# Kernel optimization log

Hardware: AMD Instinct MI355X
Metric: run time of the kernel (lower is better)

## Reference

```python
import jax, jax.numpy as jnp
import numpy as np

B, T, S, E = 32, 32, 8, 512
H, D, FF, NL = 8, 64, 2048, 4
AEMB, NACT = 64, 18
L = T * S            # qlen = 256
MEM = 256
KLEN = L + MEM       # 512


def _ln(x, g, b, eps=1e-5):
    m = jnp.mean(x, -1, keepdims=True)
    v = jnp.mean(jnp.square(x - m), -1, keepdims=True)
    return (x - m) * jax.lax.rsqrt(v + eps) * g + b


def _rel_shift(bd):
    # bd: [qlen, klen, B, H] -- TransformerXL rel-shift trick
    q, k, b, h = bd.shape
    bd = jnp.pad(bd, ((0, 0), (1, 0), (0, 0), (0, 0)))
    return bd.reshape(k + 1, q, b, h)[1:].reshape(q, k, b, h)


def setup_inputs() -> dict:
    key = jax.random.key(0)
    ks = jax.random.split(key, 20)
    s = 0.02  # weight init scale
    x = jax.random.normal(ks[0], (B, T, S, E), jnp.float32)
    action = jax.random.randint(ks[1], (B, T), 0, NACT, dtype=jnp.int32)
    i = jnp.arange(L)[:, None]
    j = jnp.arange(KLEN)[None, :]
    attn_mask = j > (i + MEM)                      # True = masked (causal w/ memory)
    positions = jnp.arange(KLEN - 1, -1, -1, dtype=jnp.int32)  # TXL descending positions
    mems = jax.random.normal(ks[2], (NL, MEM, B, E), jnp.float32) * 0.1
    return {
        'x': x, 'action': action, 'attn_mask': attn_mask, 'positions': positions,
        'mems': mems,
        'act_emb': jax.random.normal(ks[3], (NACT, AEMB), jnp.float32) * s,
        'stem_w1': jax.random.normal(ks[4], (E + AEMB, E), jnp.float32) * s,
        'stem_ln1_g': jnp.ones((E,), jnp.float32), 'stem_ln1_b': jnp.zeros((E,), jnp.float32),
        'stem_w2': jax.random.normal(ks[5], (E, E), jnp.float32) * s,
        'stem_ln2_g': jnp.ones((E,), jnp.float32), 'stem_ln2_b': jnp.zeros((E,), jnp.float32),
        'lnf_g': jnp.ones((E,), jnp.float32), 'lnf_b': jnp.zeros((E,), jnp.float32),
        'u_bias': jax.random.normal(ks[6], (H, D), jnp.float32) * s,
        'v_bias': jax.random.normal(ks[7], (H, D), jnp.float32) * s,
        'Wqkv': jax.random.normal(ks[8], (NL, E, 3 * H * D), jnp.float32) * s,
        'Wr': jax.random.normal(ks[9], (NL, E, H * D), jnp.float32) * s,
        'Wo': jax.random.normal(ks[10], (NL, H * D, E), jnp.float32) * s,
        'ln1_g': jnp.ones((NL, E), jnp.float32), 'ln1_b': jnp.zeros((NL, E), jnp.float32),
        'W1': jax.random.normal(ks[11], (NL, E, FF), jnp.float32) * s,
        'b1': jnp.zeros((NL, FF), jnp.float32),
        'W2': jax.random.normal(ks[12], (NL, FF, E), jnp.float32) * s,
        'b2': jnp.zeros((NL, E), jnp.float32),
        'ln2_g': jnp.ones((NL, E), jnp.float32), 'ln2_b': jnp.zeros((NL, E), jnp.float32),
    }


def reference(x, action, attn_mask, positions, mems, act_emb,
              stem_w1, stem_ln1_g, stem_ln1_b, stem_w2, stem_ln2_g, stem_ln2_b,
              lnf_g, lnf_b, u_bias, v_bias, Wqkv, Wr, Wo,
              ln1_g, ln1_b, W1, b1, W2, b2, ln2_g, ln2_b):
    Bv, Tv, Sv, Ev = x.shape
    Hh, Dd = u_bias.shape
    qlen = Tv * Sv
    # --- stem (StateMixer, concat type) ---
    xs = x.reshape(Bv, qlen, Ev).transpose(1, 0, 2)                # [L,B,E] time-major
    a = act_emb[action]                                            # [B,T,AEMB]
    a = jnp.repeat(a, Sv, axis=1).transpose(1, 0, 2)               # [L,B,AEMB]
    h = jnp.concatenate([xs, a], -1) @ stem_w1
    h = jax.nn.relu(_ln(h, stem_ln1_g, stem_ln1_b))
    h = _ln(h @ stem_w2, stem_ln2_g, stem_ln2_b)
    feats = _ln(h, lnf_g, lnf_b, eps=1e-6)
    # --- sinusoidal positional encoding of relative positions ---
    pf = positions.astype(jnp.float32)
    inv = 1.0 / (10000.0 ** (jnp.arange(0, Ev, 2, dtype=jnp.float32) / Ev))
    ang = pf[:, None] * inv[None, :]
    pos_emb = jnp.concatenate([jnp.sin(ang), jnp.cos(ang)], -1)    # [KLEN,E]
    scale = 1.0 / np.sqrt(Dd)
    out = feats
    for l in range(Wqkv.shape[0]):
        cat = jnp.concatenate([mems[l], out], 0)                   # [klen,B,E]
        klen = cat.shape[0]
        q, k, v = jnp.split(cat @ Wqkv[l], 3, -1)
        q = q[-qlen:].reshape(qlen, Bv, Hh, Dd)
        k = k.reshape(klen, Bv, Hh, Dd)
        v = v.reshape(klen, Bv, Hh, Dd)
        r = (pos_emb @ Wr[l]).reshape(klen, Hh, Dd)
        AC = jnp.einsum('ibhd,jbhd->ijbh', q + u_bias, k)
        BD = _rel_shift(jnp.einsum('ibhd,jhd->ijbh', q + v_bias, r))
        score = (AC + BD) * scale
        score = jnp.where(attn_mask[:, :, None, None], jnp.float32(-1e30), score)
        attn = jax.nn.softmax(score, axis=1)
        ao = jnp.einsum('ijbh,jbhd->ibhd', attn, v).reshape(qlen, Bv, Hh * Dd) @ Wo[l]
        h1 = _ln(out + ao, ln1_g[l], ln1_b[l])
        ff = jax.nn.relu(h1 @ W1[l] + b1[l]) @ W2[l] + b2[l]
        out = _ln(h1 + ff, ln2_g[l], ln2_b[l])
    return out.transpose(1, 0, 2).reshape(Bv, Tv, Sv, Ev)
```

## Files before the change

### kernel.cpp

```cpp
#include <hip/hip_runtime.h>


typedef __attribute__((ext_vector_type(8))) short bf8_t;
typedef __attribute__((ext_vector_type(4))) float f4_t;
typedef __attribute__((ext_vector_type(16))) float fx16;

__device__ __forceinline__ ushort f2bf(float f) {
    uint u = __float_as_uint(f);
    u += 0x7FFFu + ((u >> 16) & 1u);
    return (ushort)(u >> 16);
}
__device__ __forceinline__ float b2f(ushort h) {
    return __uint_as_float(((uint)h) << 16);
}
__device__ __forceinline__ void gload16(const void* g, void* l) {
    __builtin_amdgcn_global_load_lds((const __attribute__((address_space(1))) void*)g,
                                     (__attribute__((address_space(3))) void*)l, 16, 0, 0);
}
__device__ __forceinline__ void xcd_tiles(int& mt, int& nt) {
    const int gx = gridDim.x;
    const int flat = (int)blockIdx.y * gx + (int)blockIdx.x;
    const int q = (gx * gridDim.y) >> 3;
    const int swz = (flat & 7) * q + (flat >> 3);
    nt = swz % gx;
    mt = swz / gx;
}

__device__ __forceinline__ void mma32_step(const ushort* __restrict__ As,
                                           const ushort* __restrict__ Bs,
                                           int rowA0, int colB0,
                                           int l31, int hi, fx16 acc[2][2])
{
#pragma unroll
    for (int kk = 0; kk < 4; ++kk) {
        bf8_t av[2], bv[2];
#pragma unroll
        for (int i = 0; i < 2; ++i) {
            const int row = rowA0 + i * 32 + l31;
            const int ch = (kk * 2 + hi) ^ (row & 7);
            av[i] = *(const bf8_t*)(As + row * 64 + ch * 8);
        }
#pragma unroll
        for (int j = 0; j < 2; ++j) {
            const int row = colB0 + j * 32 + l31;
            const int ch = (kk * 2 + hi) ^ (row & 7);
            bv[j] = *(const bf8_t*)(Bs + row * 64 + ch * 8);
        }
#pragma unroll
        for (int i = 0; i < 2; ++i)
#pragma unroll
            for (int j = 0; j < 2; ++j)
                acc[i][j] = __builtin_amdgcn_mfma_f32_32x32x16_bf16(av[i], bv[j], acc[i][j], 0, 0, 0);
    }
}

template<bool BIAS, bool RELU, bool OUTBF>
__global__ __launch_bounds__(256)
void gemm_bf(const ushort* __restrict__ A, int lda,
             const ushort* __restrict__ Bt, int ldb,
             const float* __restrict__ bias,
             void* __restrict__ Cp, int ldc,
             int M, int N, int K)
{
    __shared__ __align__(16) ushort sh[17408];
    ushort* As = sh;
    ushort* Bs = sh + 8192;
    const int t = threadIdx.x;
    const int w = t >> 6, lane = t & 63;
    const int wr = w >> 1, wc = w & 1;
    const int l31 = lane & 31, hi = lane >> 5;
    int mt, nt; xcd_tiles(mt, nt);
    const int m0 = mt * 128, n0 = nt * 128;

    const int srow = w * 8 + (lane >> 3);
    const int gchunk = (lane & 7) ^ (srow & 7);
    const ushort* Ag = A + (size_t)(m0 + srow) * lda + gchunk * 8;
    const ushort* Bg = Bt + (size_t)(n0 + srow) * ldb + gchunk * 8;
    ushort* Asw = As + w * 512;
    ushort* Bsw = Bs + w * 512;

    fx16 acc[2][2];
#pragma unroll
    for (int i = 0; i < 2; ++i)
#pragma unroll
        for (int j = 0; j < 2; ++j)
#pragma unroll
            for (int r = 0; r < 16; ++r) acc[i][j][r] = 0.f;

    for (int k0 = 0; k0 < K; k0 += 64) {
#pragma unroll
        for (int c = 0; c < 4; ++c) {
            gload16(Ag + (size_t)c * 32 * lda, Asw + c * 2048);
            gload16(Bg + (size_t)c * 32 * ldb, Bsw + c * 2048);
        }
        Ag += 64; Bg += 64;
        __syncthreads();
        mma32_step(As, Bs, wr * 64, wc * 64, l31, hi, acc);
        __syncthreads();
    }
    const int crow0 = wr * 64, ccol0 = wc * 64;
    if (OUTBF) {
        ushort* Cs = sh;
#pragma unroll
        for (int i = 0; i < 2; ++i)
#pragma unroll
            for (int j = 0; j < 2; ++j) {
                const int colb = ccol0 + j * 32 + l31;
                float bb = BIAS ? bias[n0 + colb] : 0.f;
                fx16 v = acc[i][j];
#pragma unroll
                for (int r = 0; r < 16; ++r) {
                    float o = v[r] + bb;
                    if (RELU) o = fmaxf(o, 0.f);
                    const int rw = crow0 + i * 32 + (r & 3) + 8 * (r >> 2) + 4 * hi;
                    Cs[rw * 136 + colb] = f2bf(o);
                }
            }
        __syncthreads();
        const int orow = t >> 1, oc0 = (t & 1) * 64;
        ushort* dst = (ushort*)Cp + (size_t)(m0 + orow) * ldc + n0 + oc0;
#pragma unroll
        for (int u = 0; u < 8; ++u)
            *(bf8_t*)(dst + u * 8) = *(const bf8_t*)(Cs + orow * 136 + oc0 + u * 8);
    } else {
        float* C = (float*)Cp;
#pragma unroll
        for (int i = 0; i < 2; ++i)
#pragma unroll
            for (int j = 0; j < 2; ++j) {
                const int colb = n0 + ccol0 + j * 32 + l31;
                float bb = BIAS ? bias[colb] : 0.f;
                fx16 v = acc[i][j];
#pragma unroll
                for (int r = 0; r < 16; ++r) {
                    float o = v[r] + bb;
                    if (RELU) o = fmaxf(o, 0.f);
                    const int rw = crow0 + i * 32 + (r & 3) + 8 * (r >> 2) + 4 * hi;
                    C[(size_t)(m0 + rw) * ldc + colb] = o;
                }
            }
    }
}

__global__ __launch_bounds__(256)
void gemm_r4(const ushort* __restrict__ A, const ushort* __restrict__ WrT,
             ushort* __restrict__ R4)
{
    __shared__ __align__(16) ushort sh[17408];
    ushort* As = sh;
    ushort* Bs = sh + 8192;
    const int t = threadIdx.x;
    const int w = t >> 6, lane = t & 63;
    const int wr = w >> 1, wc = w & 1;
    const int l31 = lane & 31, hi = lane >> 5;
    const int m0 = blockIdx.y * 128, n0 = blockIdx.x * 128;
    const ushort* Bt = WrT + (size_t)blockIdx.z * 262144;
    ushort* Cp = R4 + (size_t)blockIdx.z * 262144;

    const int srow = w * 8 + (lane >> 3);
    const int gchunk = (lane & 7) ^ (srow & 7);
    const ushort* Ag = A + (size_t)(m0 + srow) * 512 + gchunk * 8;
    const ushort* Bg = Bt + (size_t)(n0 + srow) * 512 + gchunk * 8;
    ushort* Asw = As + w * 512;
    ushort* Bsw = Bs + w * 512;

    fx16 acc[2][2];
#pragma unroll
    for (int i = 0; i < 2; ++i)
#pragma unroll
        for (int j = 0; j < 2; ++j)
#pragma unroll
            for (int r = 0; r < 16; ++r) acc[i][j][r] = 0.f;

    for (int k0 = 0; k0 < 512; k0 += 64) {
#pragma unroll
        for (int c = 0; c < 4; ++c) {
            gload16(Ag + (size_t)c * 32 * 512, Asw + c * 2048);
            gload16(Bg + (size_t)c * 32 * 512, Bsw + c * 2048);
        }
        Ag += 64; Bg += 64;
        __syncthreads();
        mma32_step(As, Bs, wr * 64, wc * 64, l31, hi, acc);
        __syncthreads();
    }
    const int crow0 = wr * 64, ccol0 = wc * 64;
    ushort* Cs = sh;
#pragma unroll
    for (int i = 0; i < 2; ++i)
#pragma unroll
        for (int j = 0; j < 2; ++j) {
            const int colb = ccol0 + j * 32 + l31;
            fx16 v = acc[i][j];
#pragma unroll
            for (int r = 0; r < 16; ++r) {
                const int rw = crow0 + i * 32 + (r & 3) + 8 * (r >> 2) + 4 * hi;
                Cs[rw * 136 + colb] = f2bf(v[r]);
            }
        }
    __syncthreads();
    const int orow = t >> 1, oc0 = (t & 1) * 64;
    ushort* dst = Cp + (size_t)(m0 + orow) * 512 + n0 + oc0;
#pragma unroll
    for (int u = 0; u < 8; ++u)
        *(bf8_t*)(dst + u * 8) = *(const bf8_t*)(Cs + orow * 136 + oc0 + u * 8);
}

__global__ __launch_bounds__(256)
void gemm_qkv2(const ushort* __restrict__ Acur, const ushort* __restrict__ Amem,
               const ushort* __restrict__ wqkvT_l,
               ushort* __restrict__ qout, ushort* __restrict__ kvout)
{
    __shared__ __align__(16) ushort sh[17408];
    ushort* As = sh;
    ushort* Bs = sh + 8192;
    const int t = threadIdx.x;
    const int w = t >> 6, lane = t & 63;
    const int wr = w >> 1, wc = w & 1;
    const int l31 = lane & 31, hi = lane >> 5;
    int mt, nt; xcd_tiles(mt, nt);
    const int m0 = mt * 128;

    const ushort* A;
    const ushort* Bt;
    ushort* base; size_t ldc2;
    if (nt < 12) {
        const int n0 = nt * 128;
        A = Acur;
        Bt = wqkvT_l + (size_t)n0 * 512;
        if (n0 < 512) { base = qout + n0; ldc2 = 512; }
        else          { base = kvout + (size_t)8192 * 1024 + (n0 - 512); ldc2 = 1024; }
    } else {
        const int n0 = (nt - 12) * 128;
        A = Amem;
        Bt = wqkvT_l + (size_t)(512 + n0) * 512;
        base = kvout + n0; ldc2 = 1024;
    }

    const int srow = w * 8 + (lane >> 3);
    const int gchunk = (lane & 7) ^ (srow & 7);
    const ushort* Ag = A + (size_t)(m0 + srow) * 512 + gchunk * 8;
    const ushort* Bg = Bt + (size_t)srow * 512 + gchunk * 8;
    ushort* Asw = As + w * 512;
    ushort* Bsw = Bs + w * 512;

    fx16 acc[2][2];
#pragma unroll
    for (int i = 0; i < 2; ++i)
#pragma unroll
        for (int j = 0; j < 2; ++j)
#pragma unroll
            for (int r = 0; r < 16; ++r) acc[i][j][r] = 0.f;

    for (int k0 = 0; k0 < 512; k0 += 64) {
#pragma unroll
        for (int c = 0; c < 4; ++c) {
            gload16(Ag + (size_t)c * 32 * 512, Asw + c * 2048);
            gload16(Bg + (size_t)c * 32 * 512, Bsw + c * 2048);
        }
        Ag += 64; Bg += 64;
        __syncthreads();
        mma32_step(As, Bs, wr * 64, wc * 64, l31, hi, acc);
        __syncthreads();
    }
    const int crow0 = wr * 64, ccol0 = wc * 64;
    ushort* Cs = sh;
#pragma unroll
    for (int i = 0; i < 2; ++i)
#pragma unroll
        for (int j = 0; j < 2; ++j) {
            const int colb = ccol0 + j * 32 + l31;
            fx16 v = acc[i][j];
#pragma unroll
            for (int r = 0; r < 16; ++r) {
                const int rw = crow0 + i * 32 + (r & 3) + 8 * (r >> 2) + 4 * hi;
                Cs[rw * 136 + colb] = f2bf(v[r]);
            }
        }
    __syncthreads();
    const int orow = t >> 1, oc0 = (t & 1) * 64;
    ushort* dst = base + (size_t)(m0 + orow) * ldc2 + oc0;
#pragma unroll
    for (int u = 0; u < 8; ++u)
        *(bf8_t*)(dst + u * 8) = *(const bf8_t*)(Cs + orow * 136 + oc0 + u * 8);
}

template<bool BIAS>
__global__ __launch_bounds__(256)
void gemm_sk(const ushort* __restrict__ A, int lda,
             const ushort* __restrict__ Bt, int ldb,
             const float* __restrict__ bias,
             float* __restrict__ C0, float* __restrict__ C1, int ldc, int KH)
{
    __shared__ __align__(16) ushort sh[16384];
    ushort* As = sh;
    ushort* Bs = sh + 8192;
    const int t = threadIdx.x;
    const int w = t >> 6, lane = t & 63;
    const int wr = w >> 1, wc = w & 1;
    const int l31 = lane & 31, hi = lane >> 5;
    int mt, nt; xcd_tiles(mt, nt);
    const int m0 = mt * 128, n0 = nt * 128;
    const int z = blockIdx.z;
    A += (size_t)z * KH; Bt += (size_t)z * KH;
    float* C = z ? C1 : C0;

    const int srow = w * 8 + (lane >> 3);
    const int gchunk = (lane & 7) ^ (srow & 7);
    const ushort* Ag = A + (size_t)(m0 + srow) * lda + gchunk * 8;
    const ushort* Bg = Bt + (size_t)(n0 + srow) * ldb + gchunk * 8;
    ushort* Asw = As + w * 512;
    ushort* Bsw = Bs + w * 512;

    fx16 acc[2][2];
#pragma unroll
    for (int i = 0; i < 2; ++i)
#pragma unroll
        for (int j = 0; j < 2; ++j)
#pragma unroll
            for (int r = 0; r < 16; ++r) acc[i][j][r] = 0.f;

    for (int k0 = 0; k0 < KH; k0 += 64) {
#pragma unroll
        for (int c = 0; c < 4; ++c) {
            gload16(Ag + (size_t)c * 32 * lda, Asw + c * 2048);
            gload16(Bg + (size_t)c * 32 * ldb, Bsw + c * 2048);
        }
        Ag += 64; Bg += 64;
        __syncthreads();
        mma32_step(As, Bs, wr * 64, wc * 64, l31, hi, acc);
        __syncthreads();
    }
    const int crow0 = wr * 64, ccol0 = wc * 64;
#pragma unroll
    for (int i = 0; i < 2; ++i)
#pragma unroll
        for (int j = 0; j < 2; ++j) {
            const int colb = n0 + ccol0 + j * 32 + l31;
            float bb = (BIAS && z == 0) ? bias[colb] : 0.f;
            fx16 v = acc[i][j];
#pragma unroll
            for (int r = 0; r < 16; ++r) {
                const int rw = crow0 + i * 32 + (r & 3) + 8 * (r >> 2) + 4 * hi;
                C[(size_t)(m0 + rw) * ldc + colb] = v[r] + bb;
            }
        }
}

template<int RMODE, bool TROUT>
__global__ __launch_bounds__(256)
void ln_k(const float* __restrict__ X, const float* __restrict__ X2,
          const void* __restrict__ Rp,
          const float* __restrict__ g, const float* __restrict__ bt,
          float* __restrict__ Yf, ushort* __restrict__ Yb,
          float eps, int do_relu)
{
    const int row  = blockIdx.x * 4 + (threadIdx.x >> 6);
    const int lane = threadIdx.x & 63;
    const float* xp = X + (size_t)row * 512 + lane * 8;
    float4 x0 = *(const float4*)xp, x1 = *(const float4*)(xp + 4);
    float v[8] = {x0.x, x0.y, x0.z, x0.w, x1.x, x1.y, x1.z, x1.w};
    if (RMODE == 3) {
        const float* p2 = X2 + (size_t)row * 512 + lane * 8;
        float4 a0 = *(const float4*)p2, a1 = *(const float4*)(p2 + 4);
        v[0] += a0.x; v[1] += a0.y; v[2] += a0.z; v[3] += a0.w;
        v[4] += a1.x; v[5] += a1.y; v[6] += a1.z; v[7] += a1.w;
        const ushort* rp = (const ushort*)Rp + (size_t)row * 512 + lane * 8;
        ushort4 r0 = *(const ushort4*)rp, r1 = *(const ushort4*)(rp + 4);
        v[0] += b2f(r0.x); v[1] += b2f(r0.y); v[2] += b2f(r0.z); v[3] += b2f(r0.w);
        v[4] += b2f(r1.x); v[5] += b2f(r1.y); v[6] += b2f(r1.z); v[7] += b2f(r1.w);
    }
    float s = 0.f;
#pragma unroll
    for (int i = 0; i < 8; ++i) s += v[i];
#pragma unroll
    for (int m = 1; m < 64; m <<= 1) s += __shfl_xor(s, m);
    float mean = s * (1.f / 512.f);
    float q = 0.f;
#pragma unroll
    for (int i = 0; i < 8; ++i) { float d = v[i] - mean; q = fmaf(d, d, q); }
#pragma unroll
    for (int m = 1; m < 64; m <<= 1) q += __shfl_xor(q, m);
    float rstd = rsqrtf(q * (1.f / 512.f) + eps);
    float4 g0 = *(const float4*)(g + lane * 8), g1 = *(const float4*)(g + lane * 8 + 4);
    float4 c0 = *(const float4*)(bt + lane * 8), c1 = *(const float4*)(bt + lane * 8 + 4);
    float gv[8] = {g0.x, g0.y, g0.z, g0.w, g1.x, g1.y, g1.z, g1.w};
    float bv[8] = {c0.x, c0.y, c0.z, c0.w, c1.x, c1.y, c1.z, c1.w};
    float o[8];
#pragma unroll
    for (int i = 0; i < 8; ++i) {
        o[i] = (v[i] - mean) * rstd * gv[i] + bv[i];
        if (do_relu) o[i] = fmaxf(o[i], 0.f);
    }
    if (Yf) {
        float* yp;
        if (TROUT) {
            const int bq = row & 31, lq = row >> 5;
            yp = Yf + ((size_t)bq * 256 + lq) * 512 + lane * 8;
        } else {
            yp = Yf + (size_t)row * 512 + lane * 8;
        }
        *(float4*)yp       = make_float4(o[0], o[1], o[2], o[3]);
        *(float4*)(yp + 4) = make_float4(o[4], o[5], o[6], o[7]);
    }
    if (Yb) {
        ushort* yp = Yb + (size_t)row * 512 + lane * 8;
        ushort4 w0, w1;
        w0.x = f2bf(o[0]); w0.y = f2bf(o[1]); w0.z = f2bf(o[2]); w0.w = f2bf(o[3]);
        w1.x = f2bf(o[4]); w1.y = f2bf(o[5]); w1.z = f2bf(o[6]); w1.w = f2bf(o[7]);
        *(ushort4*)yp       = w0;
        *(ushort4*)(yp + 4) = w1;
    }
}

__global__ __launch_bounds__(256)
void ln_stem2(const float* __restrict__ X, const float* __restrict__ X2,
              const float* __restrict__ g1, const float* __restrict__ b1,
              const float* __restrict__ g2, const float* __restrict__ b2,
              ushort* __restrict__ Yb)
{
    const int row  = blockIdx.x * 4 + (threadIdx.x >> 6);
    const int lane = threadIdx.x & 63;
    const float* xp = X + (size_t)row * 512 + lane * 8;
    const float* ap = X2 + (size_t)row * 512 + lane * 8;
    float4 x0 = *(const float4*)xp, x1 = *(const float4*)(xp + 4);
    float4 a0 = *(const float4*)ap, a1 = *(const float4*)(ap + 4);
    float v[8] = {x0.x + a0.x, x0.y + a0.y, x0.z + a0.z, x0.w + a0.w,
                  x1.x + a1.x, x1.y + a1.y, x1.z + a1.z, x1.w + a1.w};
    float s = 0.f;
#pragma unroll
    for (int i = 0; i < 8; ++i) s += v[i];
#pragma unroll
    for (int m = 1; m < 64; m <<= 1) s += __shfl_xor(s, m);
    float mean = s * (1.f / 512.f);
    float q = 0.f;
#pragma unroll
    for (int i = 0; i < 8; ++i) { float d = v[i] - mean; q = fmaf(d, d, q); }
#pragma unroll
    for (int m = 1; m < 64; m <<= 1) q += __shfl_xor(q, m);
    float rstd = rsqrtf(q * (1.f / 512.f) + 1e-5f);
#pragma unroll
    for (int i = 0; i < 8; ++i)
        v[i] = (v[i] - mean) * rstd * g1[lane * 8 + i] + b1[lane * 8 + i];
    s = 0.f;
#pragma unroll
    for (int i = 0; i < 8; ++i) s += v[i];
#pragma unroll
    for (int m = 1; m < 64; m <<= 1) s += __shfl_xor(s, m);
    mean = s * (1.f / 512.f);
    q = 0.f;
#pragma unroll
    for (int i = 0; i < 8; ++i) { float d = v[i] - mean; q = fmaf(d, d, q); }
#pragma unroll
    for (int m = 1; m < 64; m <<= 1) q += __shfl_xor(q, m);
    rstd = rsqrtf(q * (1.f / 512.f) + 1e-6f);
    float o[8];
#pragma unroll
    for (int i = 0; i < 8; ++i)
        o[i] = (v[i] - mean) * rstd * g2[lane * 8 + i] + b2[lane * 8 + i];
    ushort* yb = Yb + (size_t)row * 512 + lane * 8;
    ushort4 w0, w1;
    w0.x = f2bf(o[0]); w0.y = f2bf(o[1]); w0.z = f2bf(o[2]); w0.w = f2bf(o[3]);
    w1.x = f2bf(o[4]); w1.y = f2bf(o[5]); w1.z = f2bf(o[6]); w1.w = f2bf(o[7]);
    *(ushort4*)yb       = w0;
    *(ushort4*)(yb + 4) = w1;
}

__global__ __launch_bounds__(256)
void wtrans_all(const float* __restrict__ sw1, const float* __restrict__ sw2,
                const float* __restrict__ Wqkv, const float* __restrict__ Wr,
                const float* __restrict__ Wo, const float* __restrict__ W1w,
                const float* __restrict__ W2w,
                ushort* __restrict__ w1t, ushort* __restrict__ w2t,
                ushort* __restrict__ wqkvT, ushort* __restrict__ wrT,
                ushort* __restrict__ woT, ushort* __restrict__ w1T,
                ushort* __restrict__ w2T,
                const float* __restrict__ mems, ushort* __restrict__ memsb4,
                int do_conv,
                ushort* __restrict__ pe,
                const float* __restrict__ x, const int* __restrict__ action,
                const float* __restrict__ act_emb, ushort* __restrict__ xcat)
{
    int id = (int)blockIdx.x;
    if (do_conv) {
        if (id < 8192) {
            int i = (id * 256 + threadIdx.x) * 8;
            float4 v0 = *(const float4*)(mems + i);
            float4 v1 = *(const float4*)(mems + i + 4);
            bf8_t o8;
            o8[0] = (short)f2bf(v0.x); o8[1] = (short)f2bf(v0.y);
            o8[2] = (short)f2bf(v0.z); o8[3] = (short)f2bf(v0.w);
            o8[4] = (short)f2bf(v1.x); o8[5] = (short)f2bf(v1.y);
            o8[6] = (short)f2bf(v1.z); o8[7] = (short)f2bf(v1.w);
            *(bf8_t*)(memsb4 + i) = o8;
            return;
        }
        id -= 8192;
    }
    if (id < 1024) {
        int idx = id * 256 + threadIdx.x;
        int j = idx >> 9, c = idx & 511;
        float pf = (float)(511 - j);
        int i2 = (c < 256) ? c : c - 256;
        float inv = expf(-(float)i2 * 0.03597789207803197f);
        float ang = pf * inv;
        pe[idx] = f2bf((c < 256) ? sinf(ang) : cosf(ang));
        return;
    }
    id -= 1024;
    if (id < 18432) {
        int idx = id * 256 + threadIdx.x;
        int n = idx / 576, e = idx - n * 576;
        int l = n >> 5, b = n & 31;
        float v;
        if (e < 512) v = x[((size_t)b * 256 + l) * 512 + e];
        else         v = act_emb[action[b * 32 + (l >> 3)] * 64 + (e - 512)];
        xcat[idx] = f2bf(v);
        return;
    }
    id -= 18432;
    const float* in; ushort* out; int K, N, nx, bz = 0;
    if (id < 72) { in = sw1; out = w1t; K = 576; N = 512; nx = 8; }
    else if ((id -= 72) < 64) { in = sw2; out = w2t; K = 512; N = 512; nx = 8; }
    else if ((id -= 64) < 768) { in = Wqkv; out = wqkvT; K = 512; N = 1536; nx = 24; bz = id / 192; id -= bz * 192; }
    else if ((id -= 768) < 256) { in = Wr; out = wrT; K = 512; N = 512; nx = 8; bz = id / 64; id -= bz * 64; }
    else if ((id -= 256) < 256) { in = Wo; out = woT; K = 512; N = 512; nx = 8; bz = id / 64; id -= bz * 64; }
    else if ((id -= 256) < 1024) { in = W1w; out = w1T; K = 512; N = 2048; nx = 32; bz = id / 256; id -= bz * 256; }
    else { id -= 1024; in = W2w; out = w2T; K = 2048; N = 512; nx = 8; bz = id / 256; id -= bz * 256; }
    const int bx = id % nx, by = id / nx;
    __shared__ float tl[64][65];
    const size_t bo = (size_t)bz * K * N;
    const float* inp = in + bo;
    ushort* outp = out + bo;
    const int k0 = by * 64, n0 = bx * 64;
    const int tx4 = (threadIdx.x & 15) * 4, ty = threadIdx.x >> 4;
#pragma unroll
    for (int p2 = 0; p2 < 4; ++p2) {
        const int row = p2 * 16 + ty;
        float4 v = *(const float4*)(inp + (size_t)(k0 + row) * N + n0 + tx4);
        tl[row][tx4] = v.x; tl[row][tx4 + 1] = v.y;
        tl[row][tx4 + 2] = v.z; tl[row][tx4 + 3] = v.w;
    }
    __syncthreads();
    const int nn = threadIdx.x >> 3, kk = (threadIdx.x & 7) * 8;
#pragma unroll
    for (int p2 = 0; p2 < 2; ++p2) {
        const int n = p2 * 32 + nn;
        bf8_t o8;
#pragma unroll
        for (int e = 0; e < 8; ++e) o8[e] = (short)f2bf(tl[kk + e][n]);
        *(bf8_t*)(outp + (size_t)(n0 + n) * K + k0 + kk) = o8;
    }
}

__global__ void convk(const float* __restrict__ in, ushort* __restrict__ out)
{
    int i = (blockIdx.x * 256 + threadIdx.x) * 4;
    float4 v = *(const float4*)(in + i);
    ushort4 o;
    o.x = f2bf(v.x); o.y = f2bf(v.y); o.z = f2bf(v.z); o.w = f2bf(v.w);
    *(ushort4*)(out + i) = o;
}

__global__ __launch_bounds__(512)
void attn_mfma(const ushort* __restrict__ q,
               const ushort* __restrict__ kv,
               const ushort* __restrict__ rb,
               const float* __restrict__ ub, const float* __restrict__ vb,
               ushort* __restrict__ ao)
{
    __shared__ __align__(16) ushort Ks[64][72];
    __shared__ __align__(16) ushort Vs[64][72];
    __shared__ __align__(16) ushort Rs[192][72];
    __shared__ __align__(16) ushort Ps[8][16][72];
    const int t = threadIdx.x;
    const int wv = t >> 6, lane = t & 63;
    const int lc = lane & 15, lr = lane >> 4;
    const int p = (int)blockIdx.x;
    const int b = (p & 7) * 4 + (p >> 7);
    const int hi2 = (p >> 3) & 15;
    const int h = hi2 >> 1, ihalf = hi2 & 1;
    const int i0 = ihalf << 7;
    const int iw = i0 + wv * 16;

    bf8_t au[2], aw[2];
#pragma unroll
    for (int kk = 0; kk < 2; ++kk) {
        const ushort* qp = q + ((size_t)(iw + lc) * 32 + b) * 512 + h * 64 + kk * 32 + lr * 8;
        bf8_t q8 = *(const bf8_t*)qp;
        const float* up = ub + h * 64 + kk * 32 + lr * 8;
        const float* vp = vb + h * 64 + kk * 32 + lr * 8;
#pragma unroll
        for (int e = 0; e < 8; ++e) {
            float qf = b2f((ushort)q8[e]);
            au[kk][e] = (short)f2bf(qf + up[e]);
            aw[kk][e] = (short)f2bf(qf + vp[e]);
        }
    }

    const int jl = t >> 3, d0 = (t & 7) * 8;
    const int vrow = ((t >> 3) & 7) * 8 + wv;
    const int vswz = ((((vrow >> 3) ^ (t & 7)) & 7) << 3) + (vrow & 7);

    f4_t o[4];
#pragma unroll
    for (int d = 0; d < 4; ++d) o[d] = (f4_t){0.f, 0.f, 0.f, 0.f};
    float mrun[4] = {-3.0e38f, -3.0e38f, -3.0e38f, -3.0e38f};
    float lrun[4] = {0.f, 0.f, 0.f, 0.f};

    {
        *(bf8_t*)&Ks[jl][d0] = *(const bf8_t*)(kv + ((size_t)jl * 32 + b) * 1024 + h * 64 + d0);
        bf8_t vv = *(const bf8_t*)(kv + ((size_t)vrow * 32 + b) * 1024 + 512 + h * 64 + d0);
#pragma unroll
        for (int e = 0; e < 8; ++e) Vs[d0 + e][vswz] = (ushort)vv[e];
        const int rbase0 = 128 - i0;
#pragma unroll
        for (int p2 = 0; p2 < 3; ++p2) {
            const int jr = min(rbase0 + p2 * 64 + jl, 511);
            *(bf8_t*)&Rs[p2 * 64 + jl][d0] = *(const bf8_t*)(rb + (size_t)jr * 512 + h * 64 + d0);
        }
    }
    __syncthreads();

    const int njt = ihalf ? 8 : 6;
    for (int jt = 0; jt < njt; ++jt) {
        const int j0 = jt << 6;
        bf8_t pk, pv, pr;
        const bool pfq = (jt + 1 < njt);
        if (pfq) {
            const int j0n = j0 + 64;
            pk = *(const bf8_t*)(kv + ((size_t)(j0n + jl) * 32 + b) * 1024 + h * 64 + d0);
            pv = *(const bf8_t*)(kv + ((size_t)(j0n + vrow) * 32 + b) * 1024 + 512 + h * 64 + d0);
            const int jr = min(j0n - i0 + 256 + jl, 511);
            pr = *(const bf8_t*)(rb + (size_t)jr * 512 + h * 64 + d0);
        }
        if (j0 <= iw + 271) {
            f4_t acf[4], bdf[5];
#pragma unroll
            for (int jj = 0; jj < 4; ++jj) acf[jj] = (f4_t){0.f, 0.f, 0.f, 0.f};
#pragma unroll
            for (int fj = 0; fj < 5; ++fj) bdf[fj] = (f4_t){0.f, 0.f, 0.f, 0.f};
            __builtin_amdgcn_s_setprio(1);
#pragma unroll
            for (int jj = 0; jj < 4; ++jj)
#pragma unroll
                for (int kk = 0; kk < 2; ++kk) {
                    bf8_t kf = *(const bf8_t*)&Ks[jj * 16 + lc][kk * 32 + lr * 8];
                    acf[jj] = __builtin_amdgcn_mfma_f32_16x16x32_bf16(au[kk], kf, acf[jj], 0, 0, 0);
                }
            const int rboff = 112 - wv * 16;
#pragma unroll
            for (int fj = 0; fj < 5; ++fj) {
                const int lbase = rboff + fj * 16;
                const int prow = ((jt + (lbase >> 6)) % 3) * 64 + (lbase & 63) + lc;
#pragma unroll
                for (int kk = 0; kk < 2; ++kk) {
                    bf8_t rf = *(const bf8_t*)&Rs[prow][kk * 32 + lr * 8];
                    bdf[fj] = __builtin_amdgcn_mfma_f32_16x16x32_bf16(aw[kk], rf, bdf[fj], 0, 0, 0);
                }
            }
            __builtin_amdgcn_s_setprio(0);
            float pm[4][4];
            float mt[4] = {-3.0e38f, -3.0e38f, -3.0e38f, -3.0e38f};
            const int jbase = j0 + lc - iw - 256;
#pragma unroll
            for (int rg = 0; rg < 4; ++rg) {
                const int il = lr * 4 + rg;
                const int srcl = (lane & 48) | ((lc + 15 - il) & 15);
                float shf[5];
#pragma unroll
                for (int fj = 0; fj < 5; ++fj) shf[fj] = __shfl(bdf[fj][rg], srcl, 64);
#pragma unroll
                for (int jj = 0; jj < 4; ++jj) {
                    float bd = (lc > il) ? shf[jj + 1] : shf[jj];
                    float s = (acf[jj][rg] + bd) * 0.125f;
                    if (jbase + jj * 16 > il) s = -1e30f;
                    pm[jj][rg] = s;
                    mt[rg] = fmaxf(mt[rg], s);
                }
            }
#pragma unroll
            for (int rg = 0; rg < 4; ++rg)
#pragma unroll
                for (int mm = 1; mm < 16; mm <<= 1)
                    mt[rg] = fmaxf(mt[rg], __shfl_xor(mt[rg], mm, 64));
            const bool within = (mt[0] <= mrun[0] + 8.f) & (mt[1] <= mrun[1] + 8.f) &
                                (mt[2] <= mrun[2] + 8.f) & (mt[3] <= mrun[3] + 8.f);
            const bool skip_rescale = __all(within);
            float corr[4] = {1.f, 1.f, 1.f, 1.f};
            if (!skip_rescale) {
#pragma unroll
                for (int rg = 0; rg < 4; ++rg) {
                    float mnew = fmaxf(mrun[rg], mt[rg]);
                    corr[rg] = __expf(mrun[rg] - mnew);
                    mrun[rg] = mnew;
                }
            }
            float ps4[4] = {0.f, 0.f, 0.f, 0.f};
#pragma unroll
            for (int jj = 0; jj < 4; ++jj)
#pragma unroll
                for (int rg = 0; rg < 4; ++rg) {
                    float pp = __expf(pm[jj][rg] - mrun[rg]);
                    ps4[rg] += pp;
                    Ps[wv][lr * 4 + rg][jj * 16 + lc] = f2bf(pp);
                }
#pragma unroll
            for (int rg = 0; rg < 4; ++rg)
                lrun[rg] = lrun[rg] * corr[rg] + ps4[rg];
            if (!skip_rescale) {
                float c0 = __shfl(corr[0], (lc >> 2) << 4, 64);
                float c1 = __shfl(corr[1], (lc >> 2) << 4, 64);
                float c2 = __shfl(corr[2], (lc >> 2) << 4, 64);
                float c3 = __shfl(corr[3], (lc >> 2) << 4, 64);
                float myc = (lc & 2) ? ((lc & 1) ? c3 : c2) : ((lc & 1) ? c1 : c0);
#pragma unroll
                for (int db = 0; db < 4; ++db)
#pragma unroll
                    for (int rg = 0; rg < 4; ++rg) o[db][rg] *= myc;
            }
            __builtin_amdgcn_s_setprio(1);
#pragma unroll
            for (int kb = 0; kb < 2; ++kb) {
                bf8_t pf = *(const bf8_t*)&Ps[wv][lc][kb * 32 + lr * 8];
#pragma unroll
                for (int db = 0; db < 4; ++db) {
                    const int vr = db * 16 + lc;
                    bf8_t vf = *(const bf8_t*)&Vs[vr][((kb * 4 + lr) ^ ((vr >> 3) & 7)) * 8];
                    o[db] = __builtin_amdgcn_mfma_f32_16x16x32_bf16(vf, pf, o[db], 0, 0, 0);
                }
            }
            __builtin_amdgcn_s_setprio(0);
        }
        __syncthreads();
        if (pfq) {
            *(bf8_t*)&Ks[jl][d0] = pk;
#pragma unroll
            for (int e = 0; e < 8; ++e) Vs[d0 + e][vswz] = (ushort)pv[e];
            const int phys = (jt % 3) * 64 + jl;
            *(bf8_t*)&Rs[phys][d0] = pr;
        }
        __syncthreads();
    }
    float i4[4];
#pragma unroll
    for (int rg = 0; rg < 4; ++rg) {
#pragma unroll
        for (int mm = 1; mm < 16; mm <<= 1)
            lrun[rg] += __shfl_xor(lrun[rg], mm, 64);
        i4[rg] = 1.f / lrun[rg];
    }
    float s0 = __shfl(i4[0], (lc >> 2) << 4, 64);
    float s1 = __shfl(i4[1], (lc >> 2) << 4, 64);
    float s2 = __shfl(i4[2], (lc >> 2) << 4, 64);
    float s3 = __shfl(i4[3], (lc >> 2) << 4, 64);
    float myi = (lc & 2) ? ((lc & 1) ? s3 : s2) : ((lc & 1) ? s1 : s0);
#pragma unroll
    for (int db = 0; db < 4; ++db)
#pragma unroll
        for (int rg = 0; rg < 4; ++rg)
            Ps[wv][lc][db * 16 + lr * 4 + rg] = f2bf(o[db][rg] * myi);
    const int il2 = lane >> 2, dsg = (lane & 3) << 4;
    bf8_t e0 = *(const bf8_t*)&Ps[wv][il2][dsg];
    bf8_t e1 = *(const bf8_t*)&Ps[wv][il2][dsg + 8];
    ushort* dst = ao + ((size_t)(iw + il2) * 32 + b) * 512 + h * 64 + dsg;
    *(bf8_t*)dst = e0;
    *(bf8_t*)(dst + 8) = e1;
}

extern "C" void kernel_launch(void* const* d_in, const int* in_sizes, int n_in,
                              void* d_out, int out_size, void* d_ws, size_t ws_size,
                              hipStream_t stream)
{
    const float* x       = (const float*)d_in[0];
    const int*   action  = (const int*)d_in[1];
    const float* mems    = (const float*)d_in[4];
    const float* act_emb = (const float*)d_in[5];
    const float* stem_w1 = (const float*)d_in[6];
    const float* sln1g   = (const float*)d_in[7];
    const float* sln1b   = (const float*)d_in[8];
    const float* stem_w2 = (const float*)d_in[9];
    const float* sln2g   = (const float*)d_in[10];
    const float* sln2b   = (const float*)d_in[11];
    const float* lnfg    = (const float*)d_in[12];
    const float* lnfb    = (const float*)d_in[13];
    const float* ub      = (const float*)d_in[14];
    const float* vb      = (const float*)d_in[15];
    const float* Wqkv    = (const float*)d_in[16];
    const float* Wr      = (const float*)d_in[17];
    const float* Wo      = (const float*)d_in[18];
    const float* ln1g    = (const float*)d_in[19];
    const float* ln1b    = (const float*)d_in[20];
    const float* W1      = (const float*)d_in[21];
    const float* b1      = (const float*)d_in[22];
    const float* W2      = (const float*)d_in[23];
    const float* b2      = (const float*)d_in[24];
    const float* ln2g    = (const float*)d_in[25];
    const float* ln2b    = (const float*)d_in[26];
    float* out = (float*)d_out;

    char* W = (char*)d_ws;
    float*  cur32 = (float*) (W + 0);
    float*  g32   = (float*) (W + 16777216);
    ushort* curb  = (ushort*)(W + 33554432);
    ushort* h1b   = (ushort*)(W + 41943040);
    ushort* qb    = (ushort*)(W + 50331648);
    ushort* kvb   = (ushort*)(W + 58720256);
    ushort* peb   = (ushort*)(W + 92798976);
    ushort* wts   = (ushort*)(W + 93323264);
    ushort* rbuf4 = (ushort*)(W + 121700352);
    ushort* memsb4 = (ushort*)(W + 123797504);
    const bool big_ws = ws_size >= (size_t)123797504 + 33554432;
    ushort* xcatb = kvb;
    ushort* ff1b  = kvb;
    float*  wopart = (float*)kvb;
    ushort* memsb = (ushort*)g32;
    ushort* w1t    = wts;
    ushort* w2t    = wts + 294912;
    ushort* wqkvT  = wts + 557056;
    ushort* wrT    = wts + 3702784;
    ushort* woT    = wts + 4751360;
    ushort* w1T    = wts + 5799936;
    ushort* w2T    = wts + 9994240;

    dim3 blk(256);
    const int wt_blocks = 72 + 64 + 768 + 256 + 256 + 1024 + 1024;
    const int pro_blocks = (big_ws ? 8192 : 0) + 1024 + 18432 + wt_blocks;
    wtrans_all<<<pro_blocks, blk, 0, stream>>>(
        stem_w1, stem_w2, Wqkv, Wr, Wo, W1, W2,
        w1t, w2t, wqkvT, wrT, woT, w1T, w2T,
        mems, memsb4, big_ws ? 1 : 0,
        peb, x, action, act_emb, xcatb);
    gemm_r4<<<dim3(4, 4, 4), blk, 0, stream>>>(peb, wrT, rbuf4);

    gemm_bf<false, false, false><<<dim3(4, 64), blk, 0, stream>>>(xcatb, 576, w1t, 576, nullptr, g32, 512, 8192, 512, 576);
    ln_k<0, false><<<2048, blk, 0, stream>>>(g32, nullptr, nullptr, sln1g, sln1b, nullptr, curb, 1e-5f, 1);
    gemm_sk<false><<<dim3(4, 64, 2), blk, 0, stream>>>(curb, 512, w2t, 512, nullptr, g32, cur32, 512, 256);
    ln_stem2<<<2048, blk, 0, stream>>>(g32, cur32, sln2g, sln2b, lnfg, lnfb, curb);

    for (int l = 0; l < 4; ++l) {
        const ushort* wqkvT_l = wqkvT + (size_t)l * 786432;
        const ushort* mA;
        if (big_ws) {
            mA = memsb4 + (size_t)l * 4194304;
        } else {
            convk<<<4096, blk, 0, stream>>>(mems + (size_t)l * 4194304, memsb);
            mA = memsb;
        }
        gemm_qkv2<<<dim3(20, 64), blk, 0, stream>>>(curb, mA, wqkvT_l, qb, kvb);
        attn_mfma<<<512, dim3(512), 0, stream>>>(qb, kvb, rbuf4 + (size_t)l * 262144, ub, vb, h1b);
        gemm_sk<false><<<dim3(4, 64, 2), blk, 0, stream>>>(h1b, 512, woT + (size_t)l * 262144, 512, nullptr, g32, wopart, 512, 256);
        ln_k<3, false><<<2048, blk, 0, stream>>>(g32, wopart, curb, ln1g + l * 512, ln1b + l * 512, nullptr, h1b, 1e-5f, 0);
        gemm_bf<true, true, true><<<dim3(16, 64), blk, 0, stream>>>(h1b, 512, w1T + (size_t)l * 1048576, 512, b1 + l * 2048, ff1b, 2048, 8192, 2048, 512);
        gemm_sk<true><<<dim3(4, 64, 2), blk, 0, stream>>>(ff1b, 2048, w2T + (size_t)l * 1048576, 2048, b2 + l * 512, g32, cur32, 512, 1024);
        if (l == 3)
            ln_k<3, true><<<2048, blk, 0, stream>>>(g32, cur32, h1b, ln2g + l * 512, ln2b + l * 512, out, nullptr, 1e-5f, 0);
        else
            ln_k<3, false><<<2048, blk, 0, stream>>>(g32, cur32, h1b, ln2g + l * 512, ln2b + l * 512, nullptr, curb, 1e-5f, 0);
    }
}
```

Before: 774.6 us.

## Fold positional projection GEMM into first QKV launch and vectorize prologue conversions

Removes the separate gemm_r4 launch. The positional-embedding projection for all four layers is now computed by an extra column of 64 tiles (nt==20) in the layer-0 QKV GEMM grid. The prologue's positional-encoding and input-concatenation conversions now handle 8 elements per thread with vector loads and stores, which cuts their block count sharply. This saves one launch and fills idle CUs, but adds a branch to the QKV kernel's tile mapping that depends on the XCD swizzle behaving correctly with a 21-wide grid.

```diff
diff --git a/kernel.cpp b/kernel.cpp
--- a/kernel.cpp
+++ b/kernel.cpp
@@ -143,72 +143,11 @@
 }
 
 __global__ __launch_bounds__(256)
-void gemm_r4(const ushort* __restrict__ A, const ushort* __restrict__ WrT,
-             ushort* __restrict__ R4)
-{
-    __shared__ __align__(16) ushort sh[17408];
-    ushort* As = sh;
-    ushort* Bs = sh + 8192;
-    const int t = threadIdx.x;
-    const int w = t >> 6, lane = t & 63;
-    const int wr = w >> 1, wc = w & 1;
-    const int l31 = lane & 31, hi = lane >> 5;
-    const int m0 = blockIdx.y * 128, n0 = blockIdx.x * 128;
-    const ushort* Bt = WrT + (size_t)blockIdx.z * 262144;
-    ushort* Cp = R4 + (size_t)blockIdx.z * 262144;
-
-    const int srow = w * 8 + (lane >> 3);
-    const int gchunk = (lane & 7) ^ (srow & 7);
-    const ushort* Ag = A + (size_t)(m0 + srow) * 512 + gchunk * 8;
-    const ushort* Bg = Bt + (size_t)(n0 + srow) * 512 + gchunk * 8;
-    ushort* Asw = As + w * 512;
-    ushort* Bsw = Bs + w * 512;
-
-    fx16 acc[2][2];
-#pragma unroll
-    for (int i = 0; i < 2; ++i)
-#pragma unroll
-        for (int j = 0; j < 2; ++j)
-#pragma unroll
-            for (int r = 0; r < 16; ++r) acc[i][j][r] = 0.f;
-
-    for (int k0 = 0; k0 < 512; k0 += 64) {
-#pragma unroll
-        for (int c = 0; c < 4; ++c) {
-            gload16(Ag + (size_t)c * 32 * 512, Asw + c * 2048);
-            gload16(Bg + (size_t)c * 32 * 512, Bsw + c * 2048);
-        }
-        Ag += 64; Bg += 64;
-        __syncthreads();
-        mma32_step(As, Bs, wr * 64, wc * 64, l31, hi, acc);
-        __syncthreads();
-    }
-    const int crow0 = wr * 64, ccol0 = wc * 64;
-    ushort* Cs = sh;
-#pragma unroll
-    for (int i = 0; i < 2; ++i)
-#pragma unroll
-        for (int j = 0; j < 2; ++j) {
-            const int colb = ccol0 + j * 32 + l31;
-            fx16 v = acc[i][j];
-#pragma unroll
-            for (int r = 0; r < 16; ++r) {
-                const int rw = crow0 + i * 32 + (r & 3) + 8 * (r >> 2) + 4 * hi;
-                Cs[rw * 136 + colb] = f2bf(v[r]);
-            }
-        }
-    __syncthreads();
-    const int orow = t >> 1, oc0 = (t & 1) * 64;
-    ushort* dst = Cp + (size_t)(m0 + orow) * 512 + n0 + oc0;
-#pragma unroll
-    for (int u = 0; u < 8; ++u)
-        *(bf8_t*)(dst + u * 8) = *(const bf8_t*)(Cs + orow * 136 + oc0 + u * 8);
-}
-
-__global__ __launch_bounds__(256)
 void gemm_qkv2(const ushort* __restrict__ Acur, const ushort* __restrict__ Amem,
                const ushort* __restrict__ wqkvT_l,
-               ushort* __restrict__ qout, ushort* __restrict__ kvout)
+               ushort* __restrict__ qout, ushort* __restrict__ kvout,
+               const ushort* __restrict__ peA, const ushort* __restrict__ wrTall,
+               ushort* __restrict__ r4out)
 {
     __shared__ __align__(16) ushort sh[17408];
     ushort* As = sh;
@@ -218,19 +157,29 @@
     const int wr = w >> 1, wc = w & 1;
     const int l31 = lane & 31, hi = lane >> 5;
     int mt, nt; xcd_tiles(mt, nt);
-    const int m0 = mt * 128;
-
+
+    int m0;
     const ushort* A;
     const ushort* Bt;
     ushort* base; size_t ldc2;
-    if (nt < 12) {
+    if (nt >= 20) {
+        const int rid = mt;
+        const int rz = rid >> 4, rm = (rid >> 2) & 3, rn = rid & 3;
+        m0 = rm * 128;
+        A = peA;
+        Bt = wrTall + (size_t)rz * 262144 + (size_t)(rn * 128) * 512;
+        base = r4out + (size_t)rz * 262144 + rn * 128;
+        ldc2 = 512;
+    } else if (nt < 12) {
         const int n0 = nt * 128;
+        m0 = mt * 128;
         A = Acur;
         Bt = wqkvT_l + (size_t)n0 * 512;
         if (n0 < 512) { base = qout + n0; ldc2 = 512; }
         else          { base = kvout + (size_t)8192 * 1024 + (n0 - 512); ldc2 = 1024; }
     } else {
         const int n0 = (nt - 12) * 128;
+        m0 = mt * 128;
         A = Amem;
         Bt = wqkvT_l + (size_t)(512 + n0) * 512;
         base = kvout + n0; ldc2 = 1024;
@@ -496,28 +445,47 @@
         }
         id -= 8192;
     }
-    if (id < 1024) {
-        int idx = id * 256 + threadIdx.x;
-        int j = idx >> 9, c = idx & 511;
+    if (id < 128) {
+        int v = id * 256 + threadIdx.x;
+        int j = v >> 6, c0 = (v & 63) * 8;
         float pf = (float)(511 - j);
-        int i2 = (c < 256) ? c : c - 256;
-        float inv = expf(-(float)i2 * 0.03597789207803197f);
-        float ang = pf * inv;
-        pe[idx] = f2bf((c < 256) ? sinf(ang) : cosf(ang));
+        bf8_t o8;
+#pragma unroll
+        for (int e = 0; e < 8; ++e) {
+            int c = c0 + e;
+            int i2 = (c < 256) ? c : c - 256;
+            float inv = expf(-(float)i2 * 0.03597789207803197f);
+            float ang = pf * inv;
+            o8[e] = (short)f2bf((c < 256) ? sinf(ang) : cosf(ang));
+        }
+        *(bf8_t*)(pe + (size_t)j * 512 + c0) = o8;
         return;
     }
-    id -= 1024;
-    if (id < 18432) {
-        int idx = id * 256 + threadIdx.x;
-        int n = idx / 576, e = idx - n * 576;
+    id -= 128;
+    if (id < 2304) {
+        int v = id * 256 + threadIdx.x;
+        int n = v / 72, eg = v - n * 72;
+        int e0 = eg * 8;
         int l = n >> 5, b = n & 31;
-        float v;
-        if (e < 512) v = x[((size_t)b * 256 + l) * 512 + e];
-        else         v = act_emb[action[b * 32 + (l >> 3)] * 64 + (e - 512)];
-        xcat[idx] = f2bf(v);
+        float4 v0, v1;
+        if (e0 < 512) {
+            const float* src = x + ((size_t)b * 256 + l) * 512 + e0;
+            v0 = *(const float4*)src;
+            v1 = *(const float4*)(src + 4);
+        } else {
+            const float* src = act_emb + (size_t)action[b * 32 + (l >> 3)] * 64 + (e0 - 512);
+            v0 = *(const float4*)src;
+            v1 = *(const float4*)(src + 4);
+        }
+        bf8_t o8;
+        o8[0] = (short)f2bf(v0.x); o8[1] = (short)f2bf(v0.y);
+        o8[2] = (short)f2bf(v0.z); o8[3] = (short)f2bf(v0.w);
+        o8[4] = (short)f2bf(v1.x); o8[5] = (short)f2bf(v1.y);
+        o8[6] = (short)f2bf(v1.z); o8[7] = (short)f2bf(v1.w);
+        *(bf8_t*)(xcat + (size_t)n * 576 + e0) = o8;
         return;
     }
-    id -= 18432;
+    id -= 2304;
     const float* in; ushort* out; int K, N, nx, bz = 0;
     if (id < 72) { in = sw1; out = w1t; K = 576; N = 512; nx = 8; }
     else if ((id -= 72) < 64) { in = sw2; out = w2t; K = 512; N = 512; nx = 8; }
@@ -660,7 +628,7 @@
             }
             __builtin_amdgcn_s_setprio(0);
             float pm[4][4];
-            float mt[4] = {-3.0e38f, -3.0e38f, -3.0e38f, -3.0e38f};
+            float mt2[4] = {-3.0e38f, -3.0e38f, -3.0e38f, -3.0e38f};
             const int jbase = j0 + lc - iw - 256;
 #pragma unroll
             for (int rg = 0; rg < 4; ++rg) {
@@ -675,22 +643,22 @@
                     float s = (acf[jj][rg] + bd) * 0.125f;
                     if (jbase + jj * 16 > il) s = -1e30f;
                     pm[jj][rg] = s;
-                    mt[rg] = fmaxf(mt[rg], s);
+                    mt2[rg] = fmaxf(mt2[rg], s);
                 }
             }
 #pragma unroll
             for (int rg = 0; rg < 4; ++rg)
 #pragma unroll
                 for (int mm = 1; mm < 16; mm <<= 1)
-                    mt[rg] = fmaxf(mt[rg], __shfl_xor(mt[rg], mm, 64));
-            const bool within = (mt[0] <= mrun[0] + 8.f) & (mt[1] <= mrun[1] + 8.f) &
-                                (mt[2] <= mrun[2] + 8.f) & (mt[3] <= mrun[3] + 8.f);
+                    mt2[rg] = fmaxf(mt2[rg], __shfl_xor(mt2[rg], mm, 64));
+            const bool within = (mt2[0] <= mrun[0] + 8.f) & (mt2[1] <= mrun[1] + 8.f) &
+                                (mt2[2] <= mrun[2] + 8.f) & (mt2[3] <= mrun[3] + 8.f);
             const bool skip_rescale = __all(within);
             float corr[4] = {1.f, 1.f, 1.f, 1.f};
             if (!skip_rescale) {
 #pragma unroll
                 for (int rg = 0; rg < 4; ++rg) {
-                    float mnew = fmaxf(mrun[rg], mt[rg]);
+                    float mnew = fmaxf(mrun[rg], mt2[rg]);
                     corr[rg] = __expf(mrun[rg] - mnew);
                     mrun[rg] = mnew;
                 }
@@ -824,13 +792,12 @@
 
     dim3 blk(256);
     const int wt_blocks = 72 + 64 + 768 + 256 + 256 + 1024 + 1024;
-    const int pro_blocks = (big_ws ? 8192 : 0) + 1024 + 18432 + wt_blocks;
+    const int pro_blocks = (big_ws ? 8192 : 0) + 128 + 2304 + wt_blocks;
     wtrans_all<<<pro_blocks, blk, 0, stream>>>(
         stem_w1, stem_w2, Wqkv, Wr, Wo, W1, W2,
         w1t, w2t, wqkvT, wrT, woT, w1T, w2T,
         mems, memsb4, big_ws ? 1 : 0,
         peb, x, action, act_emb, xcatb);
-    gemm_r4<<<dim3(4, 4, 4), blk, 0, stream>>>(peb, wrT, rbuf4);
 
     gemm_bf<false, false, false><<<dim3(4, 64), blk, 0, stream>>>(xcatb, 576, w1t, 576, nullptr, g32, 512, 8192, 512, 576);
     ln_k<0, false><<<2048, blk, 0, stream>>>(g32, nullptr, nullptr, sln1g, sln1b, nullptr, curb, 1e-5f, 1);
@@ -846,7 +813,10 @@
             convk<<<4096, blk, 0, stream>>>(mems + (size_t)l * 4194304, memsb);
             mA = memsb;
         }
-        gemm_qkv2<<<dim3(20, 64), blk, 0, stream>>>(curb, mA, wqkvT_l, qb, kvb);
+        if (l == 0)
+            gemm_qkv2<<<dim3(21, 64), blk, 0, stream>>>(curb, mA, wqkvT_l, qb, kvb, peb, wrT, rbuf4);
+        else
+            gemm_qkv2<<<dim3(20, 64), blk, 0, stream>>>(curb, mA, wqkvT_l, qb, kvb, peb, wrT, rbuf4);
         attn_mfma<<<512, dim3(512), 0, stream>>>(qb, kvb, rbuf4 + (size_t)l * 262144, ub, vb, h1b);
         gemm_sk<false><<<dim3(4, 64, 2), blk, 0, stream>>>(h1b, 512, woT + (size_t)l * 262144, 512, nullptr, g32, wopart, 512, 256);
         ln_k<3, false><<<2048, blk, 0, stream>>>(g32, wopart, curb, ln1g + l * 512, ln1b + l * 512, nullptr, h1b, 1e-5f, 0);
```

Result: no change. 763.6 us (-1.4%).
